# Optimization experiments

Hardware: AMD Instinct MI355X
Metric: run time of the kernel (lower is better)

## Reference

```python
import jax, jax.numpy as jnp
import numpy as np

B, T, D = 2, 2048, 1024
NH, NKV, HD = 16, 4, 64
BASE, TSL, QGI = 10000.0, 1024, 1.5
EPS = 1.1920929e-07  # torch.finfo(float32).eps used by F.rms_norm default


def _rope_cos_sin(seq_len, rd):
    # Rotary.forward with self.rd == head_dim (Attn sets rd=0 -> full rotation)
    if seq_len > TSL:  # NTK-style base rescale branch
        nb = BASE * (seq_len / TSL) ** (rd / (rd - 2))
    else:
        nb = BASE
    inv = 1.0 / nb ** (jnp.arange(0, rd, 2, dtype=jnp.float32) / rd)
    fr = jnp.arange(seq_len, dtype=jnp.float32)[:, None] * inv[None, :]
    return jnp.cos(fr)[None, :, None, :], jnp.sin(fr)[None, :, None, :]


def _apply_rope(x, cos, sin):
    h = x.shape[-1] // 2
    x1, x2 = x[..., :h], x[..., h:]
    return jnp.concatenate([x1 * cos + x2 * sin, -x1 * sin + x2 * cos], axis=-1)


def _rms_norm(x):
    return x * jax.lax.rsqrt(jnp.mean(x * x, axis=-1, keepdims=True) + EPS)


def setup_inputs() -> dict:
    key = jax.random.key(0)
    ks = jax.random.split(key, 8)
    s = jnp.float32(0.02)
    return {
        "x": jax.random.normal(ks[0], (B, T, D), jnp.float32),
        "qw": jax.random.normal(ks[1], (NH * HD, D), jnp.float32) * s,
        "kw": jax.random.normal(ks[2], (NKV * HD, D), jnp.float32) * s,
        "vw": jax.random.normal(ks[3], (NKV * HD, D), jnp.float32) * s,
        "ow": jax.random.normal(ks[4], (D, D), jnp.float32) * s,
        "ve": jax.random.normal(ks[5], (B, T, NKV * HD), jnp.float32) * s,
        "v0": jax.random.normal(ks[6], (B, T, NKV, HD), jnp.float32) * s,
        "q_gain": jnp.full((NH,), QGI, jnp.float32),
        "vr_lambda": jnp.array([0.5, 0.5], jnp.float32),
        "gate_w": jnp.zeros((NH, D), jnp.float32),      # nn.init.zeros_
        "gate_b": jnp.full((NH,), 4.0, jnp.float32),    # nn.init.constant_(4.0)
    }


def reference(x, qw, kw, vw, ow, ve, v0, q_gain, vr_lambda, gate_w, gate_b):
    # projections
    q = (x @ qw.T).reshape(B, T, NH, HD)
    k = (x @ kw.T).reshape(B, T, NKV, HD)
    v = (x @ vw.T + ve).reshape(B, T, NKV, HD)
    raw_v = v  # returned when vr=True
    v = vr_lambda[0] * v0 + vr_lambda[1] * v  # value residual
    # qk rms-norm + rope (full head dim since self.rd == 0) + per-head q gain
    q = _rms_norm(q)
    k = _rms_norm(k)
    cos, sin = _rope_cos_sin(T, HD)
    q = _apply_rope(q, cos, sin)
    k = _apply_rope(k, cos, sin)
    q = q * q_gain[None, None, :, None]
    # causal GQA attention (nh query heads share nkv kv heads)
    G = NH // NKV
    qg = q.reshape(B, T, NKV, G, HD)
    scale = 1.0 / np.sqrt(HD).astype(np.float32)
    scores = jnp.einsum('bqhgd,bkhd->bhgqk', qg, k) * scale  # [B,NKV,G,T,T]
    causal = jnp.tril(jnp.ones((T, T), bool))
    scores = jnp.where(causal[None, None, None], scores, jnp.finfo(scores.dtype).min)
    p = jax.nn.softmax(scores, axis=-1)
    y = jnp.einsum('bhgqk,bkhd->bqhgd', p, v).reshape(B, T, NH, HD)
    # gated attention output
    gate = jax.nn.sigmoid(x @ gate_w.T + gate_b)  # [B,T,NH]
    y = y * gate[..., None]
    out = y.reshape(B, T, D) @ ow.T
    return out, raw_v
```

## Files before the change

### kernel.cpp

```cpp
#include <hip/hip_runtime.h>
#include <math.h>

#define BB 2
#define TT 2048
#define DD 1024
#define NH 16
#define NKV 4
#define HD 64
#define EPSF 1.1920929e-07f
#define LOG2_NB 14.319970444065578
#define SCALE_LOG2E 0.18033688011112042f
#define FIXMAX 17.5f

typedef __attribute__((ext_vector_type(8))) short bf16x8;
typedef __attribute__((ext_vector_type(4))) float f32x4;

__device__ inline short f2bf(float f) {
    unsigned u = __builtin_bit_cast(unsigned, f);
    unsigned r = (u + 0x7fffu + ((u >> 16) & 1u)) >> 16;
    return (short)r;
}
__device__ inline float bf2f(short s) {
    unsigned u = ((unsigned)(unsigned short)s) << 16;
    return __builtin_bit_cast(float, u);
}
__device__ inline unsigned cvt_pk_bf16(float a, float b) {
    unsigned r;
    asm("v_cvt_pk_bf16_f32 %0, %1, %2" : "=v"(r) : "v"(a), "v"(b));
    return r;
}

__global__ __launch_bounds__(256) void conv_all(
    const float* __restrict__ x, const float* __restrict__ qw,
    const float* __restrict__ kw, const float* __restrict__ vw,
    const float* __restrict__ ow, const float* __restrict__ gw,
    short* __restrict__ x16, short* __restrict__ wb16, short* __restrict__ ow16)
{
    int i = blockIdx.x * 256 + threadIdx.x;
    if (i >= 1708032) {
        ((short4*)(wb16 + 1552*1024))[i - 1708032] = (short4){0,0,0,0};
        return;
    }
    const float* src; short* dst; int j;
    if (i < 1048576)      { src = x;  dst = x16;            j = i; }
    else if (i < 1310720) { src = qw; dst = wb16;           j = i - 1048576; }
    else if (i < 1376256) { src = kw; dst = wb16 + 1048576; j = i - 1310720; }
    else if (i < 1441792) { src = vw; dst = wb16 + 1310720; j = i - 1376256; }
    else if (i < 1703936) { src = ow; dst = ow16;           j = i - 1441792; }
    else                  { src = gw; dst = wb16 + 1572864; j = i - 1703936; }
    float4 v = ((const float4*)src)[j];
    short4 o;
    o.x = f2bf(v.x); o.y = f2bf(v.y); o.z = f2bf(v.z); o.w = f2bf(v.w);
    ((short4*)dst)[j] = o;
}

#define GSTAGE(buf, k0, Abase, Bbase)                                                   \
{                                                                                       \
    _Pragma("unroll")                                                                   \
    for (int i_ = 0; i_ < 2; i_++) {                                                    \
        int off = w*2048 + i_*1024;                      \
        int g = (off >> 4) + lane;                                   \
        int row = g >> 2, c = g & 3;                                                    \
        int cg = c ^ (row & 3);                                        \
        const short* ga = (Abase) + (size_t)(m0 + row)*1024 + (k0) + cg*8;              \
        __builtin_amdgcn_global_load_lds(                                               \
            (const __attribute__((address_space(1))) void*)ga,                          \
            (__attribute__((address_space(3))) void*)((char*)&As[buf][0] + off), 16, 0, 0); \
        const short* gb = (Bbase) + (size_t)(n0 + row)*1024 + (k0) + cg*8;              \
        __builtin_amdgcn_global_load_lds(                                               \
            (const __attribute__((address_space(1))) void*)gb,                          \
            (__attribute__((address_space(3))) void*)((char*)&Bs[buf][0] + off), 16, 0, 0); \
    }                                                                                   \
}

#define GEMM_MAIN_LOOP(kbeg, kend, Abase, Bbase)                                        \
    GSTAGE(0, (kbeg), (Abase), (Bbase));                                                \
    __syncthreads();                                                                    \
    for (int k0 = (kbeg); k0 < (kend); k0 += 32) {                                      \
        int cur = ((k0 - (kbeg)) >> 5) & 1;                                             \
        bf16x8 af[4], bfr[4];                                                           \
        _Pragma("unroll")                                                               \
        for (int tm = 0; tm < 4; tm++) {                                                \
            int row = wy*64 + tm*16 + lc;                                               \
            af[tm] = *(const bf16x8*)(&As[cur][0] + row*32 + ((quad*8) ^ ((row&3)*8))); \
        }                                                                               \
        _Pragma("unroll")                                                               \
        for (int tn = 0; tn < 4; tn++) {                                                \
            int row = wx*64 + tn*16 + lc;                                               \
            bfr[tn] = *(const bf16x8*)(&Bs[cur][0] + row*32 + ((quad*8) ^ ((row&3)*8))); \
        }                                                                               \
        if (k0 + 32 < (kend)) GSTAGE(cur ^ 1, k0 + 32, (Abase), (Bbase));               \
        _Pragma("unroll")                                                               \
        for (int tm = 0; tm < 4; tm++)                                                  \
            _Pragma("unroll")                                                           \
            for (int tn = 0; tn < 4; tn++)                                              \
                acc[tm][tn] = __builtin_amdgcn_mfma_f32_16x16x32_bf16(af[tm], bfr[tn], acc[tm][tn], 0, 0, 0); \
        __syncthreads();                                                                \
    }

__global__ __launch_bounds__(256, 3) void gemm_qkv_fused(
    const short* __restrict__ A, const short* __restrict__ Bmat,
    const float* __restrict__ ve, const float* __restrict__ v0,
    const float* __restrict__ q_gain, const float* __restrict__ vr_lambda,
    const float* __restrict__ gb_, float* __restrict__ gate,
    short* __restrict__ qbh, short* __restrict__ kbh, short* __restrict__ vtb,
    float* __restrict__ rawv)
{
    __shared__ short As[2][128*32];
    __shared__ short Bs[2][128*32];
    int tid = threadIdx.x;
    int w = tid >> 6, lane = tid & 63;
    int quad = lane >> 4, lc = lane & 15;
    int wy = w >> 1, wx = w & 1;
    int m0 = blockIdx.y * 128, n0 = blockIdx.x * 128;

    f32x4 acc[4][4];
    #pragma unroll
    for (int i = 0; i < 4; i++)
        #pragma unroll
        for (int j = 0; j < 4; j++) acc[i][j] = (f32x4){0.f,0.f,0.f,0.f};

    GEMM_MAIN_LOOP(0, 1024, A, Bmat);

    int hc = n0 + wx*64;
    if (hc < 1280) {
        bool isq = (hc < 1024);
        int h = isq ? (hc >> 6) : ((hc - 1024) >> 6);
        float gsc = isq ? (q_gain[h] * SCALE_LOG2E) : 1.0f;
        short* dst = isq ? qbh : kbh;
        int nhh = isq ? 16 : 4;
        float inv0 = (float)exp2((double)lc * (-LOG2_NB / 32.0));
        float inv1 = (float)exp2((double)(lc + 16) * (-LOG2_NB / 32.0));
        #pragma unroll
        for (int tm = 0; tm < 4; tm++) {
            #pragma unroll
            for (int r = 0; r < 4; r++) {
                int m = m0 + wy*64 + tm*16 + quad*4 + r;
                int b = m >> 11, t = m & (TT - 1);
                float a0 = acc[tm][0][r], a1 = acc[tm][1][r];
                float a2 = acc[tm][2][r], a3 = acc[tm][3][r];
                float ss = a0*a0 + a1*a1 + a2*a2 + a3*a3;
                ss += __shfl_xor(ss, 1);
                ss += __shfl_xor(ss, 2);
                ss += __shfl_xor(ss, 4);
                ss += __shfl_xor(ss, 8);
                float rn = rsqrtf(ss * (1.0f/64.0f) + EPSF);
                a0 *= rn; a1 *= rn; a2 *= rn; a3 *= rn;
                float sn0, cs0, sn1, cs1;
                sincosf((float)t * inv0, &sn0, &cs0);
                sincosf((float)t * inv1, &sn1, &cs1);
                float o0 = a0*cs0 + a2*sn0;
                float o1 = a1*cs1 + a3*sn1;
                float o2 = a2*cs0 - a0*sn0;
                float o3 = a3*cs1 - a1*sn1;
                size_t base = (((size_t)(b*nhh + h))*2048 + t)*64 + lc;
                dst[base +  0] = f2bf(o0 * gsc);
                dst[base + 16] = f2bf(o1 * gsc);
                dst[base + 32] = f2bf(o2 * gsc);
                dst[base + 48] = f2bf(o3 * gsc);
            }
        }
    } else if (hc < 1536) {
        int kvh = (hc - 1280) >> 6;
        float l0 = vr_lambda[0], l1 = vr_lambda[1];
        short* lbase = (w < 2) ? &As[w][0] : &Bs[w - 2][0];
        #pragma unroll
        for (int tm = 0; tm < 4; tm++) {
            #pragma unroll
            for (int r = 0; r < 4; r++) {
                int m = m0 + wy*64 + tm*16 + quad*4 + r;
                int tl = tm*16 + quad*4 + r;
                size_t off = (size_t)m*256 + kvh*64 + lc;
                #pragma unroll
                for (int tn = 0; tn < 4; tn++) {
                    int d = tn*16 + lc;
                    float val = acc[tm][tn][r] + ve[off + tn*16];
                    rawv[off + tn*16] = val;
                    lbase[d*64 + (tl ^ ((d & 7) * 8))] = f2bf(l0 * v0[off + tn*16] + l1 * val);
                }
            }
        }
        int b = m0 >> 11;
        int t0g = (m0 & 2047) + wy*64;
        short* vdst = vtb + (size_t)(b*4 + kvh)*64*2048;
        #pragma unroll
        for (int j = 0; j < 16; j++) {
            int d = quad + j*4;
            int tc = lc*4;
            short4 vv = *(const short4*)&lbase[d*64 + (tc ^ ((d & 7) * 8))];
            *(short4*)&vdst[(size_t)d*2048 + t0g + tc] = vv;
        }
    } else if (hc == 1536) {
        #pragma unroll
        for (int tm = 0; tm < 4; tm++)
            #pragma unroll
            for (int r = 0; r < 4; r++) {
                int m = m0 + wy*64 + tm*16 + quad*4 + r;
                float lg = acc[tm][0][r] + gb_[lc];
                gate[(size_t)m*16 + lc] = 1.0f / (1.0f + __expf(-lg));
            }
    }
}

__global__ __launch_bounds__(256, 4) void gemm_mfma(
    const short* __restrict__ A, const short* __restrict__ Bmat,
    float* __restrict__ C, int ldc, int klen)
{
    __shared__ short As[2][128*32];
    __shared__ short Bs[2][128*32];
    int tid = threadIdx.x;
    int w = tid >> 6, lane = tid & 63;
    int quad = lane >> 4, lc = lane & 15;
    int wy = w >> 1, wx = w & 1;
    int m0 = blockIdx.y * 128, n0 = blockIdx.x * 128;

    f32x4 acc[4][4];
    #pragma unroll
    for (int i = 0; i < 4; i++)
        #pragma unroll
        for (int j = 0; j < 4; j++) acc[i][j] = (f32x4){0.f,0.f,0.f,0.f};

    GEMM_MAIN_LOOP(0, klen, A, Bmat);

    #pragma unroll
    for (int tm = 0; tm < 4; tm++)
        #pragma unroll
        for (int r = 0; r < 4; r++) {
            int m = m0 + wy*64 + tm*16 + quad*4 + r;
            #pragma unroll
            for (int tn = 0; tn < 4; tn++) {
                int n = n0 + wx*64 + tn*16 + lc;
                C[(size_t)m*ldc + n] = acc[tm][tn][r];
            }
        }
}

__global__ __launch_bounds__(256, 4) void flash_mfma(
    const short* __restrict__ qbh, const short* __restrict__ kbh,
    const short* __restrict__ vtb, const float* __restrict__ gate,
    short* __restrict__ y16)
{
    __shared__ short Ks[2][64*64];
    __shared__ short Vt[2][64*64];
    __shared__ short Ps[4][16*64];

    int bh = blockIdx.x;
    int b = bh >> 4, h = bh & 15, kvh = h >> 2;
    int qt = 31 - blockIdx.y;
    int tid = threadIdx.x;
    int w = tid >> 6, lane = tid & 63;
    int quad = lane >> 4, lc = lane & 15;

    const short* qbase = qbh + (((size_t)bh)*2048 + qt*64 + w*16 + lc)*64;
    bf16x8 qf0 = *(const bf16x8*)(qbase + quad*8);
    bf16x8 qf1 = *(const bf16x8*)(qbase + 32 + quad*8);

    f32x4 o[4];
    #pragma unroll
    for (int i = 0; i < 4; i++) o[i] = (f32x4){0.f,0.f,0.f,0.f};
    f32x4 l4 = (f32x4){0.f,0.f,0.f,0.f};
    const bf16x8 ones = {(short)0x3F80,(short)0x3F80,(short)0x3F80,(short)0x3F80,
                         (short)0x3F80,(short)0x3F80,(short)0x3F80,(short)0x3F80};

    const size_t kbase = ((size_t)(b*4 + kvh))*2048*64;
    const size_t vbase = ((size_t)(b*4 + kvh))*64*2048;

    #define STAGE(buf, kt)                                                              \
    {                                                                                   \
        _Pragma("unroll")                                                               \
        for (int i = 0; i < 2; i++) {                                                   \
            int off = w*2048 + i*1024;                                                  \
            int g = (off >> 4) + lane;                                                  \
            int row = g >> 3, c = g & 7;                                                \
            int cg = c ^ (row & 7);                                                     \
            const short* gk = kbh + kbase + (size_t)((kt)*64 + row)*64 + cg*8;          \
            __builtin_amdgcn_global_load_lds(                                           \
                (const __attribute__((address_space(1))) void*)gk,                      \
                (__attribute__((address_space(3))) void*)((char*)Ks[buf] + off), 16, 0, 0); \
            const short* gv = vtb + vbase + (size_t)row*2048 + (kt)*64 + cg*8;          \
            __builtin_amdgcn_global_load_lds(                                           \
                (const __attribute__((address_space(1))) void*)gv,                      \
                (__attribute__((address_space(3))) void*)((char*)Vt[buf] + off), 16, 0, 0); \
        }                                                                               \
    }

    STAGE(0, 0);
    __syncthreads();

    short* ps = Ps[w];

    for (int kt = 0; kt <= qt; kt++) {
        int cur = kt & 1;
        bool diag = (kt == qt);

        bf16x8 kf0[4], kf1[4], vf0[4], vf1[4];
        #pragma unroll
        for (int kn = 0; kn < 4; kn++) {
            int row = kn*16 + lc;
            int sw = (row & 7) * 8;
            const short* kr = Ks[cur] + row*64;
            kf0[kn] = *(const bf16x8*)(kr + ((quad*8) ^ sw));
            kf1[kn] = *(const bf16x8*)(kr + ((quad*8 + 32) ^ sw));
            const short* vr = Vt[cur] + row*64;
            vf0[kn] = *(const bf16x8*)(vr + ((quad*8) ^ sw));
            vf1[kn] = *(const bf16x8*)(vr + ((quad*8 + 32) ^ sw));
        }
        if (kt < qt) STAGE(cur ^ 1, kt + 1);

        f32x4 s4[4];
        #pragma unroll
        for (int kn = 0; kn < 4; kn++) {
            f32x4 acc = (f32x4){0.f,0.f,0.f,0.f};
            acc = __builtin_amdgcn_mfma_f32_16x16x32_bf16(kf0[kn], qf0, acc, 0, 0, 0);
            acc = __builtin_amdgcn_mfma_f32_16x16x32_bf16(kf1[kn], qf1, acc, 0, 0, 0);
            s4[kn] = acc;
        }

        #pragma unroll
        for (int kn = 0; kn < 4; kn++) {
            float p0 = __builtin_amdgcn_exp2f(s4[kn][0] - FIXMAX);
            float p1 = __builtin_amdgcn_exp2f(s4[kn][1] - FIXMAX);
            float p2 = __builtin_amdgcn_exp2f(s4[kn][2] - FIXMAX);
            float p3 = __builtin_amdgcn_exp2f(s4[kn][3] - FIXMAX);
            if (diag) {
                int keyb = kn*16 + quad*4, qv = w*16 + lc;
                if (keyb + 0 > qv) p0 = 0.f;
                if (keyb + 1 > qv) p1 = 0.f;
                if (keyb + 2 > qv) p2 = 0.f;
                if (keyb + 3 > qv) p3 = 0.f;
            }
            int c = kn*4 + quad;
            int cs = c ^ ((lc & 7) << 1);
            int2 pk;
            pk.x = (int)cvt_pk_bf16(p0, p1);
            pk.y = (int)cvt_pk_bf16(p2, p3);
            *(int2*)(ps + lc*64 + cs*4) = pk;
        }
        __asm__ volatile("s_waitcnt lgkmcnt(0)" ::: "memory");
        int u0 = (0*4 + quad) ^ (lc & 7);
        int u1 = (1*4 + quad) ^ (lc & 7);
        bf16x8 pf0 = *(const bf16x8*)(ps + lc*64 + u0*8);
        bf16x8 pf1 = *(const bf16x8*)(ps + lc*64 + u1*8);

        #pragma unroll
        for (int dn = 0; dn < 4; dn++) {
            o[dn] = __builtin_amdgcn_mfma_f32_16x16x32_bf16(pf0, vf0[dn], o[dn], 0, 0, 0);
            o[dn] = __builtin_amdgcn_mfma_f32_16x16x32_bf16(pf1, vf1[dn], o[dn], 0, 0, 0);
        }
        l4 = __builtin_amdgcn_mfma_f32_16x16x32_bf16(pf0, ones, l4, 0, 0, 0);
        l4 = __builtin_amdgcn_mfma_f32_16x16x32_bf16(pf1, ones, l4, 0, 0, 0);
        __syncthreads();
    }

    #pragma unroll
    for (int r = 0; r < 4; r++) {
        int row = b*2048 + qt*64 + w*16 + quad*4 + r;
        float g = gate[(size_t)row*16 + h] / l4[r];
        #pragma unroll
        for (int dn = 0; dn < 4; dn++)
            y16[(size_t)row*1024 + h*64 + dn*16 + lc] = f2bf(o[dn][r] * g);
    }
}

extern "C" void kernel_launch(void* const* d_in, const int* in_sizes, int n_in,
                              void* d_out, int out_size, void* d_ws, size_t ws_size,
                              hipStream_t stream) {
    (void)in_sizes; (void)n_in; (void)out_size; (void)ws_size;
    const float* x  = (const float*)d_in[0];
    const float* qw = (const float*)d_in[1];
    const float* kw = (const float*)d_in[2];
    const float* vw = (const float*)d_in[3];
    const float* ow = (const float*)d_in[4];
    const float* ve = (const float*)d_in[5];
    const float* v0 = (const float*)d_in[6];
    const float* qg = (const float*)d_in[7];
    const float* vl = (const float*)d_in[8];
    const float* gw = (const float*)d_in[9];
    const float* gb = (const float*)d_in[10];

    float* out  = (float*)d_out;
    float* rawv = out + (size_t)BB*TT*DD;

    float* p    = (float*)d_ws;
    short* x16  = (short*)p;        p += 2097152;
    short* wb16 = (short*)p;        p += 851968;
    short* ow16 = (short*)p;        p += 524288;
    short* qbh  = (short*)p;        p += 2097152;
    short* kbh  = (short*)p;        p += 524288;
    short* vtb  = (short*)p;        p += 524288;
    float* gt   = p;                p += 65536;
    short* y16  = (short*)p;

    conv_all<<<6784, 256, 0, stream>>>(x, qw, kw, vw, ow, gw, x16, wb16, ow16);
    gemm_qkv_fused<<<dim3(13, 32), 256, 0, stream>>>(x16, wb16, ve, v0, qg, vl,
                                                     gb, gt, qbh, kbh, vtb, rawv);
    flash_mfma<<<dim3(32, 32), 256, 0, stream>>>(qbh, kbh, vtb, gt, y16);
    gemm_mfma<<<dim3(8, 32), 256, 0, stream>>>(y16, ow16, out, 1024, 1024);
}
```

Before: 186.1 us.

## Triple-buffer GEMM and flash loads, pair causal query tiles, swap grid order

Both GEMM kernels move from a double buffer to a three-stage LDS ring, prefetching two tiles ahead. Each step waits with an explicit vmcnt count plus a barrier instead of a full __syncthreads. The flash kernel gets the same three-stage K/V ring and has each block process a low and a high causal query tile together, which balances work across blocks and reuses each staged K/V tile for both. The grid axes are swapped so consecutive blocks walk the M dimension. In exchange, the extra LDS and registers cut occupancy (launch bounds drop to 3 and 2), and the flash grid is halved to 512 blocks.

```diff
diff --git a/kernel.cpp b/kernel.cpp
--- a/kernel.cpp
+++ b/kernel.cpp
@@ -19,10 +19,6 @@
     unsigned u = __builtin_bit_cast(unsigned, f);
     unsigned r = (u + 0x7fffu + ((u >> 16) & 1u)) >> 16;
     return (short)r;
-}
-__device__ inline float bf2f(short s) {
-    unsigned u = ((unsigned)(unsigned short)s) << 16;
-    return __builtin_bit_cast(float, u);
 }
 __device__ inline unsigned cvt_pk_bf16(float a, float b) {
     unsigned r;
@@ -54,7 +50,7 @@
     ((short4*)dst)[j] = o;
 }
 
-#define GSTAGE(buf, k0, Abase, Bbase)                                                   \
+#define GSTAGE(Abuf, Bbuf, k0, Abase, Bbase)                                            \
 {                                                                                       \
     _Pragma("unroll")                                                                   \
     for (int i_ = 0; i_ < 2; i_++) {                                                    \
@@ -65,37 +61,45 @@
         const short* ga = (Abase) + (size_t)(m0 + row)*1024 + (k0) + cg*8;              \
         __builtin_amdgcn_global_load_lds(                                               \
             (const __attribute__((address_space(1))) void*)ga,                          \
-            (__attribute__((address_space(3))) void*)((char*)&As[buf][0] + off), 16, 0, 0); \
+            (__attribute__((address_space(3))) void*)((char*)(Abuf) + off), 16, 0, 0);  \
         const short* gb = (Bbase) + (size_t)(n0 + row)*1024 + (k0) + cg*8;              \
         __builtin_amdgcn_global_load_lds(                                               \
             (const __attribute__((address_space(1))) void*)gb,                          \
-            (__attribute__((address_space(3))) void*)((char*)&Bs[buf][0] + off), 16, 0, 0); \
+            (__attribute__((address_space(3))) void*)((char*)(Bbuf) + off), 16, 0, 0);  \
     }                                                                                   \
 }
 
-#define GEMM_MAIN_LOOP(kbeg, kend, Abase, Bbase)                                        \
-    GSTAGE(0, (kbeg), (Abase), (Bbase));                                                \
-    __syncthreads();                                                                    \
-    for (int k0 = (kbeg); k0 < (kend); k0 += 32) {                                      \
-        int cur = ((k0 - (kbeg)) >> 5) & 1;                                             \
-        bf16x8 af[4], bfr[4];                                                           \
-        _Pragma("unroll")                                                               \
-        for (int tm = 0; tm < 4; tm++) {                                                \
-            int row = wy*64 + tm*16 + lc;                                               \
-            af[tm] = *(const bf16x8*)(&As[cur][0] + row*32 + ((quad*8) ^ ((row&3)*8))); \
+#define GEMM_RING_LOOP(KLEN, Abase, Bbase)                                              \
+    GSTAGE(&As[0][0], &Bs[0][0], 0,  (Abase), (Bbase));                                 \
+    GSTAGE(&As[1][0], &Bs[1][0], 32, (Abase), (Bbase));                                 \
+    {                                                                                   \
+        int steps = (KLEN) >> 5;                                                        \
+        for (int st = 0; st < steps; st++) {                                            \
+            int k0 = st << 5;                                                           \
+            int cur = st % 3;                                                           \
+            if (st < steps - 1) asm volatile("s_waitcnt vmcnt(4)\n\ts_barrier" ::: "memory"); \
+            else                asm volatile("s_waitcnt vmcnt(0)\n\ts_barrier" ::: "memory"); \
+            bf16x8 af[4], bfr[4];                                                       \
+            _Pragma("unroll")                                                           \
+            for (int tm = 0; tm < 4; tm++) {                                            \
+                int row = wy*64 + tm*16 + lc;                                           \
+                af[tm] = *(const bf16x8*)(&As[cur][0] + row*32 + ((quad*8) ^ ((row&3)*8))); \
+            }                                                                           \
+            _Pragma("unroll")                                                           \
+            for (int tn = 0; tn < 4; tn++) {                                            \
+                int row = wx*64 + tn*16 + lc;                                           \
+                bfr[tn] = *(const bf16x8*)(&Bs[cur][0] + row*32 + ((quad*8) ^ ((row&3)*8))); \
+            }                                                                           \
+            if (st + 2 < steps) {                                                       \
+                int nxt = (st + 2) % 3;                                                 \
+                GSTAGE(&As[nxt][0], &Bs[nxt][0], k0 + 64, (Abase), (Bbase));            \
+            }                                                                           \
+            _Pragma("unroll")                                                           \
+            for (int tm = 0; tm < 4; tm++)                                              \
+                _Pragma("unroll")                                                       \
+                for (int tn = 0; tn < 4; tn++)                                          \
+                    acc[tm][tn] = __builtin_amdgcn_mfma_f32_16x16x32_bf16(af[tm], bfr[tn], acc[tm][tn], 0, 0, 0); \
         }                                                                               \
-        _Pragma("unroll")                                                               \
-        for (int tn = 0; tn < 4; tn++) {                                                \
-            int row = wx*64 + tn*16 + lc;                                               \
-            bfr[tn] = *(const bf16x8*)(&Bs[cur][0] + row*32 + ((quad*8) ^ ((row&3)*8))); \
-        }                                                                               \
-        if (k0 + 32 < (kend)) GSTAGE(cur ^ 1, k0 + 32, (Abase), (Bbase));               \
-        _Pragma("unroll")                                                               \
-        for (int tm = 0; tm < 4; tm++)                                                  \
-            _Pragma("unroll")                                                           \
-            for (int tn = 0; tn < 4; tn++)                                              \
-                acc[tm][tn] = __builtin_amdgcn_mfma_f32_16x16x32_bf16(af[tm], bfr[tn], acc[tm][tn], 0, 0, 0); \
-        __syncthreads();                                                                \
     }
 
 __global__ __launch_bounds__(256, 3) void gemm_qkv_fused(
@@ -106,13 +110,13 @@
     short* __restrict__ qbh, short* __restrict__ kbh, short* __restrict__ vtb,
     float* __restrict__ rawv)
 {
-    __shared__ short As[2][128*32];
-    __shared__ short Bs[2][128*32];
+    __shared__ short As[3][128*32];
+    __shared__ short Bs[3][128*32];
     int tid = threadIdx.x;
     int w = tid >> 6, lane = tid & 63;
     int quad = lane >> 4, lc = lane & 15;
     int wy = w >> 1, wx = w & 1;
-    int m0 = blockIdx.y * 128, n0 = blockIdx.x * 128;
+    int m0 = blockIdx.x * 128, n0 = blockIdx.y * 128;
 
     f32x4 acc[4][4];
     #pragma unroll
@@ -120,7 +124,8 @@
         #pragma unroll
         for (int j = 0; j < 4; j++) acc[i][j] = (f32x4){0.f,0.f,0.f,0.f};
 
-    GEMM_MAIN_LOOP(0, 1024, A, Bmat);
+    GEMM_RING_LOOP(1024, A, Bmat);
+    __syncthreads();
 
     int hc = n0 + wx*64;
     if (hc < 1280) {
@@ -163,7 +168,8 @@
     } else if (hc < 1536) {
         int kvh = (hc - 1280) >> 6;
         float l0 = vr_lambda[0], l1 = vr_lambda[1];
-        short* lbase = (w < 2) ? &As[w][0] : &Bs[w - 2][0];
+        short* lbase = (w < 3) ? (short*)((char*)&As[0][0] + w*8192)
+                               : (short*)&Bs[0][0];
         #pragma unroll
         for (int tm = 0; tm < 4; tm++) {
             #pragma unroll
@@ -202,17 +208,17 @@
     }
 }
 
-__global__ __launch_bounds__(256, 4) void gemm_mfma(
+__global__ __launch_bounds__(256, 3) void gemm_mfma(
     const short* __restrict__ A, const short* __restrict__ Bmat,
     float* __restrict__ C, int ldc, int klen)
 {
-    __shared__ short As[2][128*32];
-    __shared__ short Bs[2][128*32];
+    __shared__ short As[3][128*32];
+    __shared__ short Bs[3][128*32];
     int tid = threadIdx.x;
     int w = tid >> 6, lane = tid & 63;
     int quad = lane >> 4, lc = lane & 15;
     int wy = w >> 1, wx = w & 1;
-    int m0 = blockIdx.y * 128, n0 = blockIdx.x * 128;
+    int m0 = blockIdx.x * 128, n0 = blockIdx.y * 128;
 
     f32x4 acc[4][4];
     #pragma unroll
@@ -220,7 +226,7 @@
         #pragma unroll
         for (int j = 0; j < 4; j++) acc[i][j] = (f32x4){0.f,0.f,0.f,0.f};
 
-    GEMM_MAIN_LOOP(0, klen, A, Bmat);
+    GEMM_RING_LOOP(klen, A, Bmat);
 
     #pragma unroll
     for (int tm = 0; tm < 4; tm++)
@@ -235,30 +241,35 @@
         }
 }
 
-__global__ __launch_bounds__(256, 4) void flash_mfma(
+__global__ __launch_bounds__(256, 2) void flash_mfma(
     const short* __restrict__ qbh, const short* __restrict__ kbh,
     const short* __restrict__ vtb, const float* __restrict__ gate,
     short* __restrict__ y16)
 {
-    __shared__ short Ks[2][64*64];
-    __shared__ short Vt[2][64*64];
-    __shared__ short Ps[4][16*64];
+    __shared__ short Ks[3][64*64];
+    __shared__ short Vt[3][64*64];
+    __shared__ short Ps[8][16*64];
 
     int bh = blockIdx.x;
     int b = bh >> 4, h = bh & 15, kvh = h >> 2;
-    int qt = 31 - blockIdx.y;
+    int j = blockIdx.y;
+    int qlo = j, qhi = 31 - j;
     int tid = threadIdx.x;
     int w = tid >> 6, lane = tid & 63;
     int quad = lane >> 4, lc = lane & 15;
 
-    const short* qbase = qbh + (((size_t)bh)*2048 + qt*64 + w*16 + lc)*64;
-    bf16x8 qf0 = *(const bf16x8*)(qbase + quad*8);
-    bf16x8 qf1 = *(const bf16x8*)(qbase + 32 + quad*8);
-
-    f32x4 o[4];
+    const short* qbaseL = qbh + (((size_t)bh)*2048 + qlo*64 + w*16 + lc)*64;
+    bf16x8 qfL0 = *(const bf16x8*)(qbaseL + quad*8);
+    bf16x8 qfL1 = *(const bf16x8*)(qbaseL + 32 + quad*8);
+    const short* qbaseH = qbh + (((size_t)bh)*2048 + qhi*64 + w*16 + lc)*64;
+    bf16x8 qfH0 = *(const bf16x8*)(qbaseH + quad*8);
+    bf16x8 qfH1 = *(const bf16x8*)(qbaseH + 32 + quad*8);
+
+    f32x4 oL[4], oH[4];
     #pragma unroll
-    for (int i = 0; i < 4; i++) o[i] = (f32x4){0.f,0.f,0.f,0.f};
-    f32x4 l4 = (f32x4){0.f,0.f,0.f,0.f};
+    for (int i = 0; i < 4; i++) { oL[i] = (f32x4){0.f,0.f,0.f,0.f}; oH[i] = (f32x4){0.f,0.f,0.f,0.f}; }
+    f32x4 lL = (f32x4){0.f,0.f,0.f,0.f};
+    f32x4 lH = (f32x4){0.f,0.f,0.f,0.f};
     const bf16x8 ones = {(short)0x3F80,(short)0x3F80,(short)0x3F80,(short)0x3F80,
                          (short)0x3F80,(short)0x3F80,(short)0x3F80,(short)0x3F80};
 
@@ -284,14 +295,61 @@
         }                                                                               \
     }
 
+    #define ATT_TILE(qf0_, qf1_, oacc, lacc, ps_, qtv)                                  \
+    {                                                                                   \
+        f32x4 s4[4];                                                                    \
+        _Pragma("unroll")                                                               \
+        for (int kn = 0; kn < 4; kn++) {                                                \
+            f32x4 a_ = (f32x4){0.f,0.f,0.f,0.f};                                        \
+            a_ = __builtin_amdgcn_mfma_f32_16x16x32_bf16(kf0[kn], qf0_, a_, 0, 0, 0);   \
+            a_ = __builtin_amdgcn_mfma_f32_16x16x32_bf16(kf1[kn], qf1_, a_, 0, 0, 0);   \
+            s4[kn] = a_;                                                                \
+        }                                                                               \
+        bool diag = (kt == (qtv));                                                      \
+        _Pragma("unroll")                                                               \
+        for (int kn = 0; kn < 4; kn++) {                                                \
+            float p0 = __builtin_amdgcn_exp2f(s4[kn][0] - FIXMAX);                      \
+            float p1 = __builtin_amdgcn_exp2f(s4[kn][1] - FIXMAX);                      \
+            float p2 = __builtin_amdgcn_exp2f(s4[kn][2] - FIXMAX);                      \
+            float p3 = __builtin_amdgcn_exp2f(s4[kn][3] - FIXMAX);                      \
+            if (diag) {                                                                 \
+                int keyb = kn*16 + quad*4, qv = w*16 + lc;                              \
+                if (keyb + 0 > qv) p0 = 0.f;                                            \
+                if (keyb + 1 > qv) p1 = 0.f;                                            \
+                if (keyb + 2 > qv) p2 = 0.f;                                            \
+                if (keyb + 3 > qv) p3 = 0.f;                                            \
+            }                                                                           \
+            int c = kn*4 + quad;                                                        \
+            int cs = c ^ ((lc & 7) << 1);                                               \
+            int2 pk;                                                                    \
+            pk.x = (int)cvt_pk_bf16(p0, p1);                                            \
+            pk.y = (int)cvt_pk_bf16(p2, p3);                                            \
+            *(int2*)((ps_) + lc*64 + cs*4) = pk;                                        \
+        }                                                                               \
+        __asm__ volatile("s_waitcnt lgkmcnt(0)" ::: "memory");                          \
+        int u0 = (0*4 + quad) ^ (lc & 7);                                               \
+        int u1 = (1*4 + quad) ^ (lc & 7);                                               \
+        bf16x8 pf0 = *(const bf16x8*)((ps_) + lc*64 + u0*8);                            \
+        bf16x8 pf1 = *(const bf16x8*)((ps_) + lc*64 + u1*8);                            \
+        _Pragma("unroll")                                                               \
+        for (int dn = 0; dn < 4; dn++) {                                                \
+            oacc[dn] = __builtin_amdgcn_mfma_f32_16x16x32_bf16(pf0, vf0[dn], oacc[dn], 0, 0, 0); \
+            oacc[dn] = __builtin_amdgcn_mfma_f32_16x16x32_bf16(pf1, vf1[dn], oacc[dn], 0, 0, 0); \
+        }                                                                               \
+        lacc = __builtin_amdgcn_mfma_f32_16x16x32_bf16(pf0, ones, lacc, 0, 0, 0);       \
+        lacc = __builtin_amdgcn_mfma_f32_16x16x32_bf16(pf1, ones, lacc, 0, 0, 0);       \
+    }
+
     STAGE(0, 0);
-    __syncthreads();
-
-    short* ps = Ps[w];
-
-    for (int kt = 0; kt <= qt; kt++) {
-        int cur = kt & 1;
-        bool diag = (kt == qt);
+    STAGE(1, 1);
+
+    short* psH = Ps[w];
+    short* psL = Ps[4 + w];
+
+    for (int kt = 0; kt <= qhi; kt++) {
+        int cur = kt % 3;
+        if (kt < qhi) asm volatile("s_waitcnt vmcnt(4)\n\ts_barrier" ::: "memory");
+        else          asm volatile("s_waitcnt vmcnt(0)\n\ts_barrier" ::: "memory");
 
         bf16x8 kf0[4], kf1[4], vf0[4], vf1[4];
         #pragma unroll
@@ -305,61 +363,26 @@
             vf0[kn] = *(const bf16x8*)(vr + ((quad*8) ^ sw));
             vf1[kn] = *(const bf16x8*)(vr + ((quad*8 + 32) ^ sw));
         }
-        if (kt < qt) STAGE(cur ^ 1, kt + 1);
-
-        f32x4 s4[4];
-        #pragma unroll
-        for (int kn = 0; kn < 4; kn++) {
-            f32x4 acc = (f32x4){0.f,0.f,0.f,0.f};
-            acc = __builtin_amdgcn_mfma_f32_16x16x32_bf16(kf0[kn], qf0, acc, 0, 0, 0);
-            acc = __builtin_amdgcn_mfma_f32_16x16x32_bf16(kf1[kn], qf1, acc, 0, 0, 0);
-            s4[kn] = acc;
-        }
-
-        #pragma unroll
-        for (int kn = 0; kn < 4; kn++) {
-            float p0 = __builtin_amdgcn_exp2f(s4[kn][0] - FIXMAX);
-            float p1 = __builtin_amdgcn_exp2f(s4[kn][1] - FIXMAX);
-            float p2 = __builtin_amdgcn_exp2f(s4[kn][2] - FIXMAX);
-            float p3 = __builtin_amdgcn_exp2f(s4[kn][3] - FIXMAX);
-            if (diag) {
-                int keyb = kn*16 + quad*4, qv = w*16 + lc;
-                if (keyb + 0 > qv) p0 = 0.f;
-                if (keyb + 1 > qv) p1 = 0.f;
-                if (keyb + 2 > qv) p2 = 0.f;
-                if (keyb + 3 > qv) p3 = 0.f;
-            }
-            int c = kn*4 + quad;
-            int cs = c ^ ((lc & 7) << 1);
-            int2 pk;
-            pk.x = (int)cvt_pk_bf16(p0, p1);
-            pk.y = (int)cvt_pk_bf16(p2, p3);
-            *(int2*)(ps + lc*64 + cs*4) = pk;
-        }
-        __asm__ volatile("s_waitcnt lgkmcnt(0)" ::: "memory");
-        int u0 = (0*4 + quad) ^ (lc & 7);
-        int u1 = (1*4 + quad) ^ (lc & 7);
-        bf16x8 pf0 = *(const bf16x8*)(ps + lc*64 + u0*8);
-        bf16x8 pf1 = *(const bf16x8*)(ps + lc*64 + u1*8);
-
-        #pragma unroll
-        for (int dn = 0; dn < 4; dn++) {
-            o[dn] = __builtin_amdgcn_mfma_f32_16x16x32_bf16(pf0, vf0[dn], o[dn], 0, 0, 0);
-            o[dn] = __builtin_amdgcn_mfma_f32_16x16x32_bf16(pf1, vf1[dn], o[dn], 0, 0, 0);
-        }
-        l4 = __builtin_amdgcn_mfma_f32_16x16x32_bf16(pf0, ones, l4, 0, 0, 0);
-        l4 = __builtin_amdgcn_mfma_f32_16x16x32_bf16(pf1, ones, l4, 0, 0, 0);
-        __syncthreads();
+        if (kt + 2 <= qhi) STAGE((kt + 2) % 3, kt + 2);
+
+        ATT_TILE(qfH0, qfH1, oH, lH, psH, qhi);
+        if (kt <= qlo) ATT_TILE(qfL0, qfL1, oL, lL, psL, qlo);
     }
 
     #pragma unroll
     for (int r = 0; r < 4; r++) {
-        int row = b*2048 + qt*64 + w*16 + quad*4 + r;
-        float g = gate[(size_t)row*16 + h] / l4[r];
-        #pragma unroll
-        for (int dn = 0; dn < 4; dn++)
-            y16[(size_t)row*1024 + h*64 + dn*16 + lc] = f2bf(o[dn][r] * g);
-    }
+        int rowH = b*2048 + qhi*64 + w*16 + quad*4 + r;
+        float gH = gate[(size_t)rowH*16 + h] / lH[r];
+        int rowL = b*2048 + qlo*64 + w*16 + quad*4 + r;
+        float gL = gate[(size_t)rowL*16 + h] / lL[r];
+        #pragma unroll
+        for (int dn = 0; dn < 4; dn++) {
+            y16[(size_t)rowH*1024 + h*64 + dn*16 + lc] = f2bf(oH[dn][r] * gH);
+            y16[(size_t)rowL*1024 + h*64 + dn*16 + lc] = f2bf(oL[dn][r] * gL);
+        }
+    }
+    #undef STAGE
+    #undef ATT_TILE
 }
 
 extern "C" void kernel_launch(void* const* d_in, const int* in_sizes, int n_in,
@@ -392,8 +415,8 @@
     short* y16  = (short*)p;
 
     conv_all<<<6784, 256, 0, stream>>>(x, qw, kw, vw, ow, gw, x16, wb16, ow16);
-    gemm_qkv_fused<<<dim3(13, 32), 256, 0, stream>>>(x16, wb16, ve, v0, qg, vl,
+    gemm_qkv_fused<<<dim3(32, 13), 256, 0, stream>>>(x16, wb16, ve, v0, qg, vl,
                                                      gb, gt, qbh, kbh, vtb, rawv);
-    flash_mfma<<<dim3(32, 32), 256, 0, stream>>>(qbh, kbh, vtb, gt, y16);
-    gemm_mfma<<<dim3(8, 32), 256, 0, stream>>>(y16, ow16, out, 1024, 1024);
-}
+    flash_mfma<<<dim3(32, 16), 256, 0, stream>>>(qbh, kbh, vtb, gt, y16);
+    gemm_mfma<<<dim3(32, 8), 256, 0, stream>>>(y16, ow16, out, 1024, 1024);
+}
```

Measured after the change: 172.3 us. 1.08x faster.
